# Kernel optimization log

Measured on AMD Instinct MI355X. Metric: run time of the kernel, lower is better.

The kernel has to match this reference:

```python
import jax, jax.numpy as jnp
import numpy as np
import math

N, S, D, BF, K, NT, NL = 4096, 64, 256, 24, 8, 64, 4096

def setup_inputs() -> dict:
    key = jax.random.key(0)
    ks = jax.random.split(key, 20)
    inp = {
        "values": jax.random.normal(ks[0], (N, S), dtype=jnp.float32),
        "kinds": jax.random.randint(ks[1], (N, S), 0, K, dtype=jnp.int32),
        "mask": jax.random.randint(ks[2], (N, S), 0, 2, dtype=jnp.int32),
        "prim_type": jax.random.randint(ks[3], (N,), 0, NT, dtype=jnp.int32),
        "layer_id": jax.random.randint(ks[4], (N,), 0, NL, dtype=jnp.int32),
        "meta": jax.random.normal(ks[5], (N, 4), dtype=jnp.float32),
        # frozen Fourier projection (sigma=8)
        "B_ff": jax.random.normal(ks[6], (1, BF), dtype=jnp.float32) * 8.0,
        # embeddings (N(0,1) like nn.Embedding default)
        "kind_emb_w": jax.random.normal(ks[7], (K, D), dtype=jnp.float32),
        "type_emb_w": jax.random.normal(ks[8], (NT, D), dtype=jnp.float32),
        "layer_emb_w": jax.random.normal(ks[9], (NL, D), dtype=jnp.float32),
        # per-kind MLPs: 2B -> D -> D
        "mlp_w1": jax.random.normal(ks[10], (K, 2 * BF, D), dtype=jnp.float32) / np.sqrt(2 * BF),
        "mlp_b1": jnp.zeros((K, D), dtype=jnp.float32),
        "mlp_w2": jax.random.normal(ks[11], (K, D, D), dtype=jnp.float32) / np.sqrt(D),
        "mlp_b2": jnp.zeros((K, D), dtype=jnp.float32),
        # fuse: 3D -> D -> D
        "fuse_w1": jax.random.normal(ks[12], (3 * D, D), dtype=jnp.float32) / np.sqrt(3 * D),
        "fuse_b1": jnp.zeros((D,), dtype=jnp.float32),
        "fuse_w2": jax.random.normal(ks[13], (D, D), dtype=jnp.float32) / np.sqrt(D),
        "fuse_b2": jnp.zeros((D,), dtype=jnp.float32),
        # meta_lin: 4 -> D
        "meta_w": jax.random.normal(ks[14], (4, D), dtype=jnp.float32) / 2.0,
        "meta_b": jnp.zeros((D,), dtype=jnp.float32),
    }
    return inp

def _gelu(x):
    return jax.nn.gelu(x, approximate=False)  # torch nn.GELU default = exact erf

def reference(values, kinds, mask, prim_type, layer_id, meta, B_ff,
              kind_emb_w, type_emb_w, layer_emb_w,
              mlp_w1, mlp_b1, mlp_w2, mlp_b2,
              fuse_w1, fuse_b1, fuse_w2, fuse_b2, meta_w, meta_b):
    n, s = values.shape
    d = kind_emb_w.shape[1]
    k_kinds = kind_emb_w.shape[0]
    # Fourier features over all N*S scalar slots -> [NS, 2B]
    y = (2.0 * math.pi) * values.reshape(-1, 1) @ B_ff
    ff = jnp.concatenate([jnp.sin(y), jnp.cos(y)], axis=-1)
    kf = kinds.reshape(-1)
    # kind-routed per-kind MLP (dispatch/combine expressed as masked combine)
    out = jnp.zeros((n * s, d), dtype=values.dtype)
    for k in range(k_kinds):
        h = _gelu(ff @ mlp_w1[k] + mlp_b1[k]) @ mlp_w2[k] + mlp_b2[k]
        out = jnp.where((kf == k)[:, None], h, out)
    h_slots = out.reshape(n, s, d) + kind_emb_w[kinds]
    m = mask.astype(values.dtype)
    h_slots = h_slots * m[..., None]
    denom = jnp.clip(m.sum(axis=1, keepdims=True), 1.0)  # [N,1]
    h_num = h_slots.sum(axis=1) / denom  # masked mean pooling -> [N,D]
    h = jnp.concatenate([h_num, type_emb_w[prim_type], layer_emb_w[layer_id]], axis=-1)
    fused = _gelu(h @ fuse_w1 + fuse_b1) @ fuse_w2 + fuse_b2
    return fused + meta @ meta_w + meta_b
```

## Files before the change

### kernel.cpp

```cpp
#include <hip/hip_runtime.h>
#include <math.h>


#define W2F_HI   0
#define W2F_LO   524288
#define W1F_HI   1048576
#define W1F_LO   1179648
#define FW1F_HI  1310720
#define FW1F_LO  1507328
#define FW2F_HI  1703936
#define FW2F_LO  1769472

#define PSTR 260

typedef __attribute__((ext_vector_type(8))) short frag;
typedef __attribute__((ext_vector_type(4))) float f32x4;

__device__ __forceinline__ unsigned short f2bf_rn(float x) {
    unsigned int u = __float_as_uint(x);
    unsigned int r = (u + 0x7fffu + ((u >> 16) & 1u)) >> 16;
    return (unsigned short)r;
}
__device__ __forceinline__ float bf2f(unsigned short h) {
    return __uint_as_float(((unsigned int)h) << 16);
}
__device__ __forceinline__ void split_bf(float x, unsigned short& h, unsigned short& l) {
    unsigned short hh = f2bf_rn(x);
    h = hh;
    l = f2bf_rn(x - bf2f(hh));
}

__device__ __forceinline__ float gelu_fast(float x) {
    float u = fabsf(x) * 0.7071067811865476f;
    float t = __builtin_amdgcn_rcpf(fmaf(0.3275911f, u, 1.0f));
    float p = fmaf(fmaf(fmaf(fmaf(1.061405429f, t, -1.453152027f), t,
                             1.421413741f), t, -0.284496736f), t, 0.254829592f) * t;
    float e = __expf(-u * u);
    float er = fmaf(-p, e, 1.0f);
    er = copysignf(er, x);
    return 0.5f * x * (1.0f + er);
}

__global__ __launch_bounds__(512) void prep_kernel(
    const float* __restrict__ w1, const float* __restrict__ w2,
    const float* __restrict__ fw1, const float* __restrict__ fw2,
    short* __restrict__ ws)
{
    int tid = blockIdx.x * 512 + threadIdx.x;
    int fid = tid >> 6, ln = tid & 63;
    if (fid >= 1792) return;
    int lr = ln & 15, kq = ln >> 4;
    float v[8];
    int dhi, dlo, dsto;
    if (fid < 1024) {
        int k = fid >> 7, kst = (fid >> 4) & 7, nt = fid & 15;
        int col = nt * 16 + lr;
        #pragma unroll
        for (int b = 0; b < 8; ++b) {
            int kg = kst * 32 + kq * 8 + b;
            v[b] = w2[(k * 256 + kg) * 256 + col];
        }
        dsto = fid * 512 + ln * 8; dhi = W2F_HI; dlo = W2F_LO;
    } else if (fid < 1280) {
        int f = fid - 1024;
        int k = f >> 5, kst = (f >> 4) & 1, nt = f & 15;
        int col = nt * 16 + lr;
        #pragma unroll
        for (int b = 0; b < 8; ++b) {
            int kg = kst * 32 + kq * 8 + b;
            v[b] = (kg < 48) ? w1[(k * 48 + kg) * 256 + col] : 0.0f;
        }
        dsto = f * 512 + ln * 8; dhi = W1F_HI; dlo = W1F_LO;
    } else if (fid < 1664) {
        int f = fid - 1280;
        int kst = f >> 4, nt = f & 15;
        int col = nt * 16 + lr;
        #pragma unroll
        for (int b = 0; b < 8; ++b) {
            int kg = kst * 32 + kq * 8 + b;
            v[b] = fw1[kg * 256 + col];
        }
        dsto = f * 512 + ln * 8; dhi = FW1F_HI; dlo = FW1F_LO;
    } else {
        int f = fid - 1664;
        int kst = f >> 4, nt = f & 15;
        int col = nt * 16 + lr;
        #pragma unroll
        for (int b = 0; b < 8; ++b) {
            int kg = kst * 32 + kq * 8 + b;
            v[b] = fw2[kg * 256 + col];
        }
        dsto = f * 512 + ln * 8; dhi = FW2F_HI; dlo = FW2F_LO;
    }
    union { unsigned short u[8]; frag f; } hu, lu;
    #pragma unroll
    for (int b = 0; b < 8; ++b) split_bf(v[b], hu.u[b], lu.u[b]);
    *(frag*)(ws + dhi + dsto) = hu.f;
    *(frag*)(ws + dlo + dsto) = lu.f;
}

__global__ __launch_bounds__(1024, 4) void mono_kernel(
    const float* __restrict__ values, const int* __restrict__ kinds,
    const int* __restrict__ mask, const float* __restrict__ B_ff,
    const float* __restrict__ b1, const short* __restrict__ wsf,
    const int* __restrict__ pt, const int* __restrict__ lid,
    const float* __restrict__ meta, const float* __restrict__ type_emb,
    const float* __restrict__ layer_emb, const float* __restrict__ b2,
    const float* __restrict__ kind_emb, const float* __restrict__ fb1,
    const float* __restrict__ fb2, const float* __restrict__ meta_w,
    const float* __restrict__ meta_b, float* __restrict__ out)
{
    __shared__ __align__(16) float pool_ls[8 * 16 * PSTR];
    __shared__ float vals_ls[1024];
    __shared__ unsigned char knd_ls[1024], msk_ls[1024];
    __shared__ unsigned short list[1152];
    __shared__ short chunk_kind[80], chunk_base[80];
    __shared__ int nch_s;
    __shared__ float b1_ls[2048];
    __shared__ float Bs_ls[24];
    __shared__ float cnt_ls[128], den_ls[16], meta_ls[64];
    __shared__ int pt_ls[16], lid_ls[16];

    const int t = threadIdx.x, blk = blockIdx.x;
    const int wv = t >> 6, ln = t & 63, lr16 = ln & 15, kq = ln >> 4;
    const int gbase = blk * 1024, rb = blk * 16;

    const short* w1f_hi  = wsf + W1F_HI;
    const short* w1f_lo  = wsf + W1F_LO;
    const short* w2f_hi  = wsf + W2F_HI;
    const short* w2f_lo  = wsf + W2F_LO;
    const short* fw1f_hi = wsf + FW1F_HI;
    const short* fw1f_lo = wsf + FW1F_LO;
    const short* fw2f_hi = wsf + FW2F_HI;
    const short* fw2f_lo = wsf + FW2F_LO;

    {
        int p = t;
        vals_ls[p] = values[gbase + p];
        knd_ls[p]  = (unsigned char)kinds[gbase + p];
        msk_ls[p]  = (unsigned char)mask[gbase + p];
    }
    #pragma unroll
    for (int i = 0; i < 2; ++i) b1_ls[t + i * 1024] = b1[t + i * 1024];
    if (t < 24) Bs_ls[t] = B_ff[t];
    if (t >= 32 && t < 48) { pt_ls[t - 32] = pt[rb + t - 32]; lid_ls[t - 32] = lid[rb + t - 32]; }
    if (t >= 64 && t < 128) meta_ls[t - 64] = meta[rb * 4 + (t - 64)];
    for (int i = t; i < 8 * 16 * PSTR; i += 1024) pool_ls[i] = 0.0f;
    __syncthreads();

    {
        int r = wv;
        int kd = knd_ls[r * 64 + ln], mk = msk_ls[r * 64 + ln];
        unsigned long long balm = __ballot(mk != 0);
        int myc = 0;
        #pragma unroll
        for (int k = 0; k < 8; ++k) {
            unsigned long long bal = __ballot(mk && (kd == k));
            int c = __popcll(bal);
            myc = (ln == k) ? c : myc;
        }
        if (ln < 8) cnt_ls[r * 8 + ln] = (float)myc;
        if (ln == 0) {
            int tot = __popcll(balm);
            den_ls[r] = 1.0f / (float)(tot > 0 ? tot : 1);
        }
    }

    if (t < 64) {
        int cnts[8];
        #pragma unroll
        for (int k = 0; k < 8; ++k) cnts[k] = 0;
        for (int c = 0; c < 16; ++c) {
            int p = c * 64 + t;
            int kd = knd_ls[p], mk = msk_ls[p];
            #pragma unroll
            for (int k = 0; k < 8; ++k) {
                unsigned long long bal = __ballot(mk && (kd == k));
                cnts[k] += __popcll(bal);
            }
        }
        int offk[8], run = 0;
        #pragma unroll
        for (int k = 0; k < 8; ++k) { offk[k] = run; run += (cnts[k] + 15) & ~15; }
        int fillk[8];
        #pragma unroll
        for (int k = 0; k < 8; ++k) fillk[k] = 0;
        const unsigned long long below = (1ull << t) - 1ull;
        for (int c = 0; c < 16; ++c) {
            int p = c * 64 + t;
            int kd = knd_ls[p], mk = msk_ls[p];
            #pragma unroll
            for (int k = 0; k < 8; ++k) {
                unsigned long long bal = __ballot(mk && (kd == k));
                if (mk && (kd == k)) {
                    int rank = __popcll(bal & below);
                    list[offk[k] + fillk[k] + rank] = (unsigned short)p;
                }
                fillk[k] += __popcll(bal);
            }
        }
        #pragma unroll
        for (int k = 0; k < 8; ++k) {
            int padded = (cnts[k] + 15) & ~15;
            for (int i = cnts[k] + t; i < padded; i += 64) list[offk[k] + i] = 0xFFFFu;
        }
        if (t == 0) {
            int ci = 0;
            #pragma unroll
            for (int k = 0; k < 8; ++k) {
                int nk = (cnts[k] + 15) >> 4;
                for (int j = 0; j < nk; ++j) {
                    chunk_kind[ci] = (short)k;
                    chunk_base[ci] = (short)(offk[k] + j * 16);
                    ++ci;
                }
            }
            nch_s = ci;
        }
    }
    __syncthreads();

    const int nch = nch_s;
    for (int m = wv; m < nch; m += 16) {
        const int k = (int)chunk_kind[m];
        const int cb = (int)chunk_base[m];
        int slot = list[cb + lr16];
        float v = vals_ls[slot & 1023];
        v = (slot == 0xFFFF) ? 0.0f : v;

        frag ah[2], al[2];
        #pragma unroll
        for (int kst = 0; kst < 2; ++kst) {
            union { unsigned short u[8]; frag f; } hu, lu;
            int jb0 = kst * 32 + kq * 8;
            #pragma unroll
            for (int b = 0; b < 8; ++b) {
                int jb = jb0 + b;
                float sv;
                if (jb < 48) {
                    int jm = (jb < 24) ? jb : jb - 24;
                    float cadd = (jb < 24) ? 0.0f : 0.25f;
                    float rev = __builtin_amdgcn_fractf(fmaf(v, Bs_ls[jm], cadd));
                    sv = __builtin_amdgcn_sinf(rev);
                } else {
                    sv = 0.0f;
                }
                split_bf(sv, hu.u[b], lu.u[b]);
            }
            ah[kst] = hu.f; al[kst] = lu.f;
        }

        int e4[4];
        #pragma unroll
        for (int r = 0; r < 4; ++r) {
            int sl = list[cb + kq * 4 + r];
            e4[r] = (sl == 0xFFFF) ? -1 : ((sl >> 6) & 15);
        }

        #pragma unroll 4
        for (int nt = 0; nt < 16; ++nt) {
            int o0 = ((k * 2 + 0) * 16 + nt) * 512 + ln * 8;
            int o1 = ((k * 2 + 1) * 16 + nt) * 512 + ln * 8;
            frag bh0 = *(const frag*)(w1f_hi + o0);
            frag bl0 = *(const frag*)(w1f_lo + o0);
            frag bh1 = *(const frag*)(w1f_hi + o1);
            frag bl1 = *(const frag*)(w1f_lo + o1);
            f32x4 acc = (f32x4)0.0f;
            acc = __builtin_amdgcn_mfma_f32_16x16x32_bf16(ah[0], bh0, acc, 0, 0, 0);
            acc = __builtin_amdgcn_mfma_f32_16x16x32_bf16(al[0], bh0, acc, 0, 0, 0);
            acc = __builtin_amdgcn_mfma_f32_16x16x32_bf16(ah[0], bl0, acc, 0, 0, 0);
            acc = __builtin_amdgcn_mfma_f32_16x16x32_bf16(ah[1], bh1, acc, 0, 0, 0);
            acc = __builtin_amdgcn_mfma_f32_16x16x32_bf16(al[1], bh1, acc, 0, 0, 0);
            acc = __builtin_amdgcn_mfma_f32_16x16x32_bf16(ah[1], bl1, acc, 0, 0, 0);
            float b1v = b1_ls[k * 256 + nt * 16 + lr16];
            #pragma unroll
            for (int r = 0; r < 4; ++r) {
                if (e4[r] >= 0) {
                    float g = gelu_fast(acc[r] + b1v);
                    atomicAdd(&pool_ls[(k * 16 + e4[r]) * PSTR + nt * 16 + lr16], g);
                }
            }
        }
    }
    __syncthreads();

    f32x4 acc = (f32x4)0.0f;

    for (int k = 0; k < 8; ++k) {
        #pragma unroll 2
        for (int kst = 0; kst < 8; ++kst) {
            const float* pp = &pool_ls[(k * 16 + lr16) * PSTR + kst * 32 + kq * 8];
            f32x4 u0 = *(const f32x4*)pp;
            f32x4 u1 = *(const f32x4*)(pp + 4);
            union { unsigned short u[8]; frag f; } hu, lu;
            #pragma unroll
            for (int b = 0; b < 4; ++b) {
                split_bf(u0[b], hu.u[b], lu.u[b]);
                split_bf(u1[b], hu.u[b + 4], lu.u[b + 4]);
            }
            frag ah = hu.f, al = lu.f;
            int bo = ((k * 8 + kst) * 16 + wv) * 512 + ln * 8;
            frag bh = *(const frag*)(w2f_hi + bo);
            frag bl = *(const frag*)(w2f_lo + bo);
            acc = __builtin_amdgcn_mfma_f32_16x16x32_bf16(ah, bh, acc, 0, 0, 0);
            acc = __builtin_amdgcn_mfma_f32_16x16x32_bf16(al, bh, acc, 0, 0, 0);
            acc = __builtin_amdgcn_mfma_f32_16x16x32_bf16(ah, bl, acc, 0, 0, 0);
        }
    }
    __syncthreads();

    float* hz = pool_ls;

    {
        int col = wv * 16 + lr16;
        float bks[8];
        #pragma unroll
        for (int k = 0; k < 8; ++k) bks[k] = b2[k * 256 + col] + kind_emb[k * 256 + col];
        #pragma unroll
        for (int r = 0; r < 4; ++r) {
            int row = kq * 4 + r;
            float hv = acc[r];
            #pragma unroll
            for (int k = 0; k < 8; ++k) hv = fmaf(cnt_ls[row * 8 + k], bks[k], hv);
            hv *= den_ls[row];
            hz[row * 256 + ((((col >> 2) ^ (row & 7)) << 2) | (col & 3))] = hv;
        }
    }
    __syncthreads();

    f32x4 az = (f32x4)0.0f;

    for (int kst = 0; kst < 24; ++kst) {
        const int row = lr16;
        union { unsigned short u[8]; frag f; } hu, lu;
        if (kst < 8) {
            int c0 = kst * 8 + kq * 2;
            f32x4 u0 = *(const f32x4*)&hz[row * 256 + ((c0 ^ (row & 7)) << 2)];
            f32x4 u1 = *(const f32x4*)&hz[row * 256 + (((c0 + 1) ^ (row & 7)) << 2)];
            #pragma unroll
            for (int b = 0; b < 4; ++b) {
                split_bf(u0[b], hu.u[b], lu.u[b]);
                split_bf(u1[b], hu.u[b + 4], lu.u[b + 4]);
            }
        } else {
            const float* eb = (kst < 16) ? type_emb : layer_emb;
            const int* ids = (kst < 16) ? pt_ls : lid_ls;
            int ko = (kst & 7) * 32 + kq * 8;
            const float* sp = eb + (size_t)ids[row] * 256 + ko;
            f32x4 u0 = *(const f32x4*)sp;
            f32x4 u1 = *(const f32x4*)(sp + 4);
            #pragma unroll
            for (int b = 0; b < 4; ++b) {
                split_bf(u0[b], hu.u[b], lu.u[b]);
                split_bf(u1[b], hu.u[b + 4], lu.u[b + 4]);
            }
        }
        frag ah = hu.f, al = lu.f;
        int bo = (kst * 16 + wv) * 512 + ln * 8;
        frag bh = *(const frag*)(fw1f_hi + bo);
        frag bl = *(const frag*)(fw1f_lo + bo);
        az = __builtin_amdgcn_mfma_f32_16x16x32_bf16(ah, bh, az, 0, 0, 0);
        az = __builtin_amdgcn_mfma_f32_16x16x32_bf16(al, bh, az, 0, 0, 0);
        az = __builtin_amdgcn_mfma_f32_16x16x32_bf16(ah, bl, az, 0, 0, 0);
    }
    __syncthreads();

    {
        int col = wv * 16 + lr16;
        float fb1v = fb1[col];
        #pragma unroll
        for (int r = 0; r < 4; ++r) {
            int row = kq * 4 + r;
            float z = gelu_fast(az[r] + fb1v);
            hz[row * 256 + ((((col >> 2) ^ (row & 7)) << 2) | (col & 3))] = z;
        }
    }
    __syncthreads();

    f32x4 ao2 = (f32x4)0.0f;

    for (int kst = 0; kst < 8; ++kst) {
        const int row = lr16;
        int c0 = kst * 8 + kq * 2;
        f32x4 u0 = *(const f32x4*)&hz[row * 256 + ((c0 ^ (row & 7)) << 2)];
        f32x4 u1 = *(const f32x4*)&hz[row * 256 + (((c0 + 1) ^ (row & 7)) << 2)];
        union { unsigned short u[8]; frag f; } hu, lu;
        #pragma unroll
        for (int b = 0; b < 4; ++b) {
            split_bf(u0[b], hu.u[b], lu.u[b]);
            split_bf(u1[b], hu.u[b + 4], lu.u[b + 4]);
        }
        frag ah = hu.f, al = lu.f;
        int bo = (kst * 16 + wv) * 512 + ln * 8;
        frag bh = *(const frag*)(fw2f_hi + bo);
        frag bl = *(const frag*)(fw2f_lo + bo);
        ao2 = __builtin_amdgcn_mfma_f32_16x16x32_bf16(ah, bh, ao2, 0, 0, 0);
        ao2 = __builtin_amdgcn_mfma_f32_16x16x32_bf16(al, bh, ao2, 0, 0, 0);
        ao2 = __builtin_amdgcn_mfma_f32_16x16x32_bf16(ah, bl, ao2, 0, 0, 0);
    }

    {
        int col = wv * 16 + lr16;
        float ob = fb2[col] + meta_b[col];
        float mw0 = meta_w[col], mw1 = meta_w[256 + col];
        float mw2 = meta_w[512 + col], mw3 = meta_w[768 + col];
        #pragma unroll
        for (int r = 0; r < 4; ++r) {
            int row = kq * 4 + r;
            float o = ao2[r] + ob;
            o = fmaf(meta_ls[row * 4 + 0], mw0, o);
            o = fmaf(meta_ls[row * 4 + 1], mw1, o);
            o = fmaf(meta_ls[row * 4 + 2], mw2, o);
            o = fmaf(meta_ls[row * 4 + 3], mw3, o);
            out[(size_t)(rb + row) * 256 + col] = o;
        }
    }
}

extern "C" void kernel_launch(void* const* d_in, const int* in_sizes, int n_in,
                              void* d_out, int out_size, void* d_ws, size_t ws_size,
                              hipStream_t stream) {
    const float* values    = (const float*)d_in[0];
    const int*   kinds     = (const int*)d_in[1];
    const int*   mask      = (const int*)d_in[2];
    const int*   prim_type = (const int*)d_in[3];
    const int*   layer_id  = (const int*)d_in[4];
    const float* meta      = (const float*)d_in[5];
    const float* B_ff      = (const float*)d_in[6];
    const float* kind_emb  = (const float*)d_in[7];
    const float* type_emb  = (const float*)d_in[8];
    const float* layer_emb = (const float*)d_in[9];
    const float* mlp_w1    = (const float*)d_in[10];
    const float* mlp_b1    = (const float*)d_in[11];
    const float* mlp_w2    = (const float*)d_in[12];
    const float* mlp_b2    = (const float*)d_in[13];
    const float* fuse_w1   = (const float*)d_in[14];
    const float* fuse_b1   = (const float*)d_in[15];
    const float* fuse_w2   = (const float*)d_in[16];
    const float* fuse_b2   = (const float*)d_in[17];
    const float* meta_w    = (const float*)d_in[18];
    const float* meta_b    = (const float*)d_in[19];

    short* ws  = (short*)d_ws;
    float* out = (float*)d_out;

    prep_kernel<<<224, 512, 0, stream>>>(mlp_w1, mlp_w2, fuse_w1, fuse_w2, ws);
    mono_kernel<<<256, 1024, 0, stream>>>(values, kinds, mask, B_ff, mlp_b1, ws,
                                          prim_type, layer_id, meta, type_emb,
                                          layer_emb, mlp_b2, kind_emb, fuse_b1,
                                          fuse_b2, meta_w, meta_b, out);
}
```

Baseline: 266.9 us.

## Split K dimension across waves for tail GEMMs with LDS atomic reduction

The three post-pooling GEMMs (W2, fuse W1, fuse W2) are repartitioned so each wave takes a slice of the reduction dimension across all output column tiles. Partial sums are combined through shared-memory atomicAdd into new staging buffers, which shortens each wave's serial dependent MFMA chain. The b1 bias moves from shared memory into per-thread registers loaded from global. The cost is many LDS atomics, 64 accumulator registers per thread, extra zeroing passes and synchronisation, plus uneven work in the fuse-W1 stage where only some waves take a second pass.

```diff
diff --git a/kernel.cpp b/kernel.cpp
--- a/kernel.cpp
+++ b/kernel.cpp
@@ -111,12 +111,12 @@
     const float* __restrict__ meta_b, float* __restrict__ out)
 {
     __shared__ __align__(16) float pool_ls[8 * 16 * PSTR];
+    __shared__ __align__(16) float hz_ls[16 * PSTR];
     __shared__ float vals_ls[1024];
     __shared__ unsigned char knd_ls[1024], msk_ls[1024];
     __shared__ unsigned short list[1152];
     __shared__ short chunk_kind[80], chunk_base[80];
     __shared__ int nch_s;
-    __shared__ float b1_ls[2048];
     __shared__ float Bs_ls[24];
     __shared__ float cnt_ls[128], den_ls[16], meta_ls[64];
     __shared__ int pt_ls[16], lid_ls[16];
@@ -134,18 +134,20 @@
     const short* fw2f_hi = wsf + FW2F_HI;
     const short* fw2f_lo = wsf + FW2F_LO;
 
+    float* z_pre   = pool_ls;
+    float* out_pre = pool_ls + 16 * PSTR;
+
     {
         int p = t;
         vals_ls[p] = values[gbase + p];
         knd_ls[p]  = (unsigned char)kinds[gbase + p];
         msk_ls[p]  = (unsigned char)mask[gbase + p];
     }
-    #pragma unroll
-    for (int i = 0; i < 2; ++i) b1_ls[t + i * 1024] = b1[t + i * 1024];
     if (t < 24) Bs_ls[t] = B_ff[t];
     if (t >= 32 && t < 48) { pt_ls[t - 32] = pt[rb + t - 32]; lid_ls[t - 32] = lid[rb + t - 32]; }
     if (t >= 64 && t < 128) meta_ls[t - 64] = meta[rb * 4 + (t - 64)];
     for (int i = t; i < 8 * 16 * PSTR; i += 1024) pool_ls[i] = 0.0f;
+    for (int i = t; i < 16 * PSTR; i += 1024) hz_ls[i] = 0.0f;
     __syncthreads();
 
     {
@@ -256,6 +258,9 @@
             int sl = list[cb + kq * 4 + r];
             e4[r] = (sl == 0xFFFF) ? -1 : ((sl >> 6) & 15);
         }
+        float b1r[16];
+        #pragma unroll
+        for (int nt = 0; nt < 16; ++nt) b1r[nt] = b1[k * 256 + nt * 16 + lr16];
 
         #pragma unroll 4
         for (int nt = 0; nt < 16; ++nt) {
@@ -272,11 +277,10 @@
             acc = __builtin_amdgcn_mfma_f32_16x16x32_bf16(ah[1], bh1, acc, 0, 0, 0);
             acc = __builtin_amdgcn_mfma_f32_16x16x32_bf16(al[1], bh1, acc, 0, 0, 0);
             acc = __builtin_amdgcn_mfma_f32_16x16x32_bf16(ah[1], bl1, acc, 0, 0, 0);
-            float b1v = b1_ls[k * 256 + nt * 16 + lr16];
             #pragma unroll
             for (int r = 0; r < 4; ++r) {
                 if (e4[r] >= 0) {
-                    float g = gelu_fast(acc[r] + b1v);
+                    float g = gelu_fast(acc[r] + b1r[nt]);
                     atomicAdd(&pool_ls[(k * 16 + e4[r]) * PSTR + nt * 16 + lr16], g);
                 }
             }
@@ -284,11 +288,16 @@
     }
     __syncthreads();
 
-    f32x4 acc = (f32x4)0.0f;
-
-    for (int k = 0; k < 8; ++k) {
-        #pragma unroll 2
-        for (int kst = 0; kst < 8; ++kst) {
+    {
+        f32x4 accA[16];
+        #pragma unroll
+        for (int nt = 0; nt < 16; ++nt) accA[nt] = (f32x4)0.0f;
+
+        const int k = wv >> 1;
+        const int kst0 = (wv & 1) * 4;
+        #pragma unroll 1
+        for (int kk = 0; kk < 4; ++kk) {
+            int kst = kst0 + kk;
             const float* pp = &pool_ls[(k * 16 + lr16) * PSTR + kst * 32 + kq * 8];
             f32x4 u0 = *(const f32x4*)pp;
             f32x4 u1 = *(const f32x4*)(pp + 4);
@@ -299,18 +308,25 @@
                 split_bf(u1[b], hu.u[b + 4], lu.u[b + 4]);
             }
             frag ah = hu.f, al = lu.f;
-            int bo = ((k * 8 + kst) * 16 + wv) * 512 + ln * 8;
-            frag bh = *(const frag*)(w2f_hi + bo);
-            frag bl = *(const frag*)(w2f_lo + bo);
-            acc = __builtin_amdgcn_mfma_f32_16x16x32_bf16(ah, bh, acc, 0, 0, 0);
-            acc = __builtin_amdgcn_mfma_f32_16x16x32_bf16(al, bh, acc, 0, 0, 0);
-            acc = __builtin_amdgcn_mfma_f32_16x16x32_bf16(ah, bl, acc, 0, 0, 0);
-        }
-    }
-    __syncthreads();
-
-    float* hz = pool_ls;
-
+            #pragma unroll
+            for (int nt = 0; nt < 16; ++nt) {
+                int bo = ((k * 8 + kst) * 16 + nt) * 512 + ln * 8;
+                frag bh = *(const frag*)(w2f_hi + bo);
+                frag bl = *(const frag*)(w2f_lo + bo);
+                accA[nt] = __builtin_amdgcn_mfma_f32_16x16x32_bf16(ah, bh, accA[nt], 0, 0, 0);
+                accA[nt] = __builtin_amdgcn_mfma_f32_16x16x32_bf16(al, bh, accA[nt], 0, 0, 0);
+                accA[nt] = __builtin_amdgcn_mfma_f32_16x16x32_bf16(ah, bl, accA[nt], 0, 0, 0);
+            }
+        }
+        #pragma unroll
+        for (int nt = 0; nt < 16; ++nt)
+            #pragma unroll
+            for (int r = 0; r < 4; ++r)
+                atomicAdd(&hz_ls[(kq * 4 + r) * PSTR + nt * 16 + lr16], accA[nt][r]);
+    }
+    __syncthreads();
+
+    for (int i = t; i < 32 * PSTR; i += 1024) pool_ls[i] = 0.0f;
     {
         int col = wv * 16 + lr16;
         float bks[8];
@@ -319,71 +335,73 @@
         #pragma unroll
         for (int r = 0; r < 4; ++r) {
             int row = kq * 4 + r;
-            float hv = acc[r];
+            float hv = hz_ls[row * PSTR + col];
             #pragma unroll
             for (int k = 0; k < 8; ++k) hv = fmaf(cnt_ls[row * 8 + k], bks[k], hv);
-            hv *= den_ls[row];
-            hz[row * 256 + ((((col >> 2) ^ (row & 7)) << 2) | (col & 3))] = hv;
-        }
-    }
-    __syncthreads();
-
-    f32x4 az = (f32x4)0.0f;
-
-    for (int kst = 0; kst < 24; ++kst) {
-        const int row = lr16;
-        union { unsigned short u[8]; frag f; } hu, lu;
-        if (kst < 8) {
-            int c0 = kst * 8 + kq * 2;
-            f32x4 u0 = *(const f32x4*)&hz[row * 256 + ((c0 ^ (row & 7)) << 2)];
-            f32x4 u1 = *(const f32x4*)&hz[row * 256 + (((c0 + 1) ^ (row & 7)) << 2)];
+            hz_ls[row * PSTR + col] = hv * den_ls[row];
+        }
+    }
+    __syncthreads();
+
+    {
+        f32x4 accB[16];
+        #pragma unroll
+        for (int nt = 0; nt < 16; ++nt) accB[nt] = (f32x4)0.0f;
+
+        #pragma unroll 1
+        for (int pass = 0; pass < 2; ++pass) {
+            if (pass == 1 && wv >= 8) break;
+            int kst = (pass == 0) ? wv : 16 + wv;
+            union { unsigned short u[8]; frag f; } hu, lu;
+            f32x4 u0, u1;
+            if (kst < 8) {
+                const float* pp = &hz_ls[lr16 * PSTR + kst * 32 + kq * 8];
+                u0 = *(const f32x4*)pp;
+                u1 = *(const f32x4*)(pp + 4);
+            } else {
+                const float* eb = (kst < 16) ? type_emb : layer_emb;
+                const int* ids = (kst < 16) ? pt_ls : lid_ls;
+                const float* sp = eb + (size_t)ids[lr16] * 256 + (kst & 7) * 32 + kq * 8;
+                u0 = *(const f32x4*)sp;
+                u1 = *(const f32x4*)(sp + 4);
+            }
             #pragma unroll
             for (int b = 0; b < 4; ++b) {
                 split_bf(u0[b], hu.u[b], lu.u[b]);
                 split_bf(u1[b], hu.u[b + 4], lu.u[b + 4]);
             }
-        } else {
-            const float* eb = (kst < 16) ? type_emb : layer_emb;
-            const int* ids = (kst < 16) ? pt_ls : lid_ls;
-            int ko = (kst & 7) * 32 + kq * 8;
-            const float* sp = eb + (size_t)ids[row] * 256 + ko;
-            f32x4 u0 = *(const f32x4*)sp;
-            f32x4 u1 = *(const f32x4*)(sp + 4);
-            #pragma unroll
-            for (int b = 0; b < 4; ++b) {
-                split_bf(u0[b], hu.u[b], lu.u[b]);
-                split_bf(u1[b], hu.u[b + 4], lu.u[b + 4]);
-            }
-        }
-        frag ah = hu.f, al = lu.f;
-        int bo = (kst * 16 + wv) * 512 + ln * 8;
-        frag bh = *(const frag*)(fw1f_hi + bo);
-        frag bl = *(const frag*)(fw1f_lo + bo);
-        az = __builtin_amdgcn_mfma_f32_16x16x32_bf16(ah, bh, az, 0, 0, 0);
-        az = __builtin_amdgcn_mfma_f32_16x16x32_bf16(al, bh, az, 0, 0, 0);
-        az = __builtin_amdgcn_mfma_f32_16x16x32_bf16(ah, bl, az, 0, 0, 0);
-    }
-    __syncthreads();
-
-    {
-        int col = wv * 16 + lr16;
-        float fb1v = fb1[col];
-        #pragma unroll
-        for (int r = 0; r < 4; ++r) {
-            int row = kq * 4 + r;
-            float z = gelu_fast(az[r] + fb1v);
-            hz[row * 256 + ((((col >> 2) ^ (row & 7)) << 2) | (col & 3))] = z;
-        }
-    }
-    __syncthreads();
-
-    f32x4 ao2 = (f32x4)0.0f;
-
-    for (int kst = 0; kst < 8; ++kst) {
-        const int row = lr16;
-        int c0 = kst * 8 + kq * 2;
-        f32x4 u0 = *(const f32x4*)&hz[row * 256 + ((c0 ^ (row & 7)) << 2)];
-        f32x4 u1 = *(const f32x4*)&hz[row * 256 + (((c0 + 1) ^ (row & 7)) << 2)];
+            frag ah = hu.f, al = lu.f;
+            #pragma unroll
+            for (int nt = 0; nt < 16; ++nt) {
+                int bo = (kst * 16 + nt) * 512 + ln * 8;
+                frag bh = *(const frag*)(fw1f_hi + bo);
+                frag bl = *(const frag*)(fw1f_lo + bo);
+                accB[nt] = __builtin_amdgcn_mfma_f32_16x16x32_bf16(ah, bh, accB[nt], 0, 0, 0);
+                accB[nt] = __builtin_amdgcn_mfma_f32_16x16x32_bf16(al, bh, accB[nt], 0, 0, 0);
+                accB[nt] = __builtin_amdgcn_mfma_f32_16x16x32_bf16(ah, bl, accB[nt], 0, 0, 0);
+            }
+        }
+        #pragma unroll
+        for (int nt = 0; nt < 16; ++nt)
+            #pragma unroll
+            for (int r = 0; r < 4; ++r)
+                atomicAdd(&z_pre[(kq * 4 + r) * PSTR + nt * 16 + lr16], accB[nt][r]);
+    }
+    __syncthreads();
+
+    for (int i = t; i < 4096; i += 1024) {
+        int row = i >> 8, col = i & 255;
+        float zp = z_pre[row * PSTR + col] + fb1[col];
+        z_pre[row * PSTR + col] = gelu_fast(zp);
+    }
+    __syncthreads();
+
+    {
+        const int kstC = wv >> 1;
+        const int nt0 = (wv & 1) * 8;
+        const float* pp = &z_pre[lr16 * PSTR + kstC * 32 + kq * 8];
+        f32x4 u0 = *(const f32x4*)pp;
+        f32x4 u1 = *(const f32x4*)(pp + 4);
         union { unsigned short u[8]; frag f; } hu, lu;
         #pragma unroll
         for (int b = 0; b < 4; ++b) {
@@ -391,29 +409,35 @@
             split_bf(u1[b], hu.u[b + 4], lu.u[b + 4]);
         }
         frag ah = hu.f, al = lu.f;
-        int bo = (kst * 16 + wv) * 512 + ln * 8;
-        frag bh = *(const frag*)(fw2f_hi + bo);
-        frag bl = *(const frag*)(fw2f_lo + bo);
-        ao2 = __builtin_amdgcn_mfma_f32_16x16x32_bf16(ah, bh, ao2, 0, 0, 0);
-        ao2 = __builtin_amdgcn_mfma_f32_16x16x32_bf16(al, bh, ao2, 0, 0, 0);
-        ao2 = __builtin_amdgcn_mfma_f32_16x16x32_bf16(ah, bl, ao2, 0, 0, 0);
-    }
-
-    {
-        int col = wv * 16 + lr16;
-        float ob = fb2[col] + meta_b[col];
-        float mw0 = meta_w[col], mw1 = meta_w[256 + col];
-        float mw2 = meta_w[512 + col], mw3 = meta_w[768 + col];
-        #pragma unroll
-        for (int r = 0; r < 4; ++r) {
-            int row = kq * 4 + r;
-            float o = ao2[r] + ob;
-            o = fmaf(meta_ls[row * 4 + 0], mw0, o);
-            o = fmaf(meta_ls[row * 4 + 1], mw1, o);
-            o = fmaf(meta_ls[row * 4 + 2], mw2, o);
-            o = fmaf(meta_ls[row * 4 + 3], mw3, o);
-            out[(size_t)(rb + row) * 256 + col] = o;
-        }
+        f32x4 accC[8];
+        #pragma unroll
+        for (int j = 0; j < 8; ++j) accC[j] = (f32x4)0.0f;
+        #pragma unroll
+        for (int j = 0; j < 8; ++j) {
+            int nt = nt0 + j;
+            int bo = (kstC * 16 + nt) * 512 + ln * 8;
+            frag bh = *(const frag*)(fw2f_hi + bo);
+            frag bl = *(const frag*)(fw2f_lo + bo);
+            accC[j] = __builtin_amdgcn_mfma_f32_16x16x32_bf16(ah, bh, accC[j], 0, 0, 0);
+            accC[j] = __builtin_amdgcn_mfma_f32_16x16x32_bf16(al, bh, accC[j], 0, 0, 0);
+            accC[j] = __builtin_amdgcn_mfma_f32_16x16x32_bf16(ah, bl, accC[j], 0, 0, 0);
+        }
+        #pragma unroll
+        for (int j = 0; j < 8; ++j)
+            #pragma unroll
+            for (int r = 0; r < 4; ++r)
+                atomicAdd(&out_pre[(kq * 4 + r) * PSTR + (nt0 + j) * 16 + lr16], accC[j][r]);
+    }
+    __syncthreads();
+
+    for (int i = t; i < 4096; i += 1024) {
+        int row = i >> 8, col = i & 255;
+        float o = out_pre[row * PSTR + col] + fb2[col] + meta_b[col];
+        o = fmaf(meta_ls[row * 4 + 0], meta_w[col], o);
+        o = fmaf(meta_ls[row * 4 + 1], meta_w[256 + col], o);
+        o = fmaf(meta_ls[row * 4 + 2], meta_w[512 + col], o);
+        o = fmaf(meta_ls[row * 4 + 3], meta_w[768 + col], o);
+        out[(size_t)(rb + row) * 256 + col] = o;
     }
 }
 
```

Measured after the change: 439.6 us. 64.7% more time.
